# Performance work log

Measured on AMD Instinct MI355X. Metric: run time of the kernel, lower is better.

Reference implementation:

```python
import jax, jax.numpy as jnp
import numpy as np

BN_EPS = 1e-5
NUM_HEADS = 4

def conv1x1_bn_silu(x, w, gamma, beta, mean, var):
    # x: (B,C,H,W), w: (Cout,Cin) -- 1x1 conv, no bias; BN in eval mode; SiLU act
    y = jnp.einsum('bchw,oc->bohw', x, w)
    g = (gamma / jnp.sqrt(var + BN_EPS))[:, None, None]
    b = (beta - mean * gamma / jnp.sqrt(var + BN_EPS))[:, None, None]
    y = y * g + b
    return y * jax.nn.sigmoid(y)

def setup_inputs() -> dict:
    key = jax.random.key(0)
    ks = jax.random.split(key, 16)
    B, H, W, C = 4, 64, 64, 256
    N = H * W
    Ckv = C // 4 * 2  # kv conv out channels = 128
    inp = {
        'x': jax.random.normal(ks[0], (B, N, C), jnp.float32),
        'y': jax.random.normal(ks[1], (B, N, C), jnp.float32),
        'H': H,
        'W': W,
        'q_w': jax.random.normal(ks[2], (C, C), jnp.float32) * (1.0 / np.sqrt(C)),
        'q_gamma': jax.random.uniform(ks[3], (C,), jnp.float32) + 0.5,
        'q_beta': jax.random.normal(ks[4], (C,), jnp.float32) * 0.1,
        'q_mean': jax.random.normal(ks[5], (C,), jnp.float32) * 0.1,
        'q_var': jax.random.uniform(ks[6], (C,), jnp.float32) + 0.5,
        'kv_w': jax.random.normal(ks[7], (Ckv, C), jnp.float32) * (1.0 / np.sqrt(C)),
        'kv_gamma': jax.random.uniform(ks[8], (Ckv,), jnp.float32) + 0.5,
        'kv_beta': jax.random.normal(ks[9], (Ckv,), jnp.float32) * 0.1,
        'kv_mean': jax.random.normal(ks[10], (Ckv,), jnp.float32) * 0.1,
        'kv_var': jax.random.uniform(ks[11], (Ckv,), jnp.float32) + 0.5,
        'proj_w': jax.random.normal(ks[12], (C, C), jnp.float32) * (1.0 / np.sqrt(C)),
        'proj_b': jax.random.normal(ks[13], (C,), jnp.float32) * 0.1,
    }
    return inp

def reference(x, y, H, W, q_w, q_gamma, q_beta, q_mean, q_var,
              kv_w, kv_gamma, kv_beta, kv_mean, kv_var, proj_w, proj_b):
    B, N, C = x.shape
    nh = NUM_HEADS
    hd = C // nh
    scale = hd ** -0.5
    x4 = x.reshape(B, C, H, W)
    y4 = y.reshape(B, C, H, W)
    # q: (B,C,H,W) -> raw reshape (B,N,nh,hd) -> (B,nh,N,hd)  (faithful to torch code)
    q = conv1x1_bn_silu(x4, q_w, q_gamma, q_beta, q_mean, q_var)
    q = q.reshape(B, N, nh, hd).transpose(0, 2, 1, 3)
    # kv: (B,C/2,H,W) -> raw reshape (B,M,2,nh,hd), M = N//4
    kv = conv1x1_bn_silu(y4, kv_w, kv_gamma, kv_beta, kv_mean, kv_var)
    kv = kv.reshape(B, -1, 2, nh, hd).transpose(2, 0, 3, 1, 4)
    k, v = kv[0], kv[1]  # (B,nh,M,hd)
    attn = jnp.einsum('bhnd,bhmd->bhnm', q * scale, k)  # (B,nh,N,M)
    att_map = jax.nn.softmax(attn, axis=-1)
    out = jnp.einsum('bhnm,bhmd->bhnd', att_map, v)  # (B,nh,N,hd)
    out = out.reshape(B, N, C)  # raw reshape, faithful to original
    out = out @ proj_w.T + proj_b
    return out
```

## Files before the change

kernel.cpp:

```cpp
#include <hip/hip_runtime.h>
#include <hip/hip_bf16.h>
#include <math.h>

#define BB 4
#define NTOK 4096
#define CC 256
#define NH 4
#define HD 64
#define CKV 128

typedef _Float16 half8 __attribute__((ext_vector_type(8)));
typedef _Float16 half4 __attribute__((ext_vector_type(4)));
typedef _Float16 half2v __attribute__((ext_vector_type(2)));
typedef float    f32x4 __attribute__((ext_vector_type(4)));
typedef unsigned int uint2v __attribute__((ext_vector_type(2)));

__device__ __forceinline__ half2v pkrtz(float a, float b) {
  return __builtin_bit_cast(half2v, __builtin_amdgcn_cvt_pkrtz(a, b));
}
__device__ __forceinline__ float exp2_fast(float x) {
  float r;
  asm("v_exp_f32 %0, %1" : "=v"(r) : "v"(x));
  return r;
}
__device__ __forceinline__ int swzi(int row, int d) {
  return row * 64 + (d ^ ((row & 7) << 3));
}
__device__ __forceinline__ int swzv(int row, int d) {
  return row * 64 + (d ^ (((row >> 1) & 7) << 3));
}
__device__ __forceinline__ f32x4 mfma16(half8 a, half8 b, f32x4 c) {
  return __builtin_amdgcn_mfma_f32_16x16x32_f16(a, b, c, 0, 0, 0);
}

__global__ __launch_bounds__(256) void pre_all(
    const float* __restrict__ x, const float* __restrict__ y,
    const float* __restrict__ qw, const float* __restrict__ qg_, const float* __restrict__ qb,
    const float* __restrict__ qm, const float* __restrict__ qv,
    const float* __restrict__ kw, const float* __restrict__ kg_, const float* __restrict__ kb,
    const float* __restrict__ km, const float* __restrict__ kvv,
    const float* __restrict__ pw,
    _Float16* __restrict__ Xt, _Float16* __restrict__ Yt,
    _Float16* __restrict__ qWh, float* __restrict__ qB2,
    _Float16* __restrict__ kWh, float* __restrict__ kB2,
    _Float16* __restrict__ pWh)
{
  const int id = blockIdx.x;
  __shared__ float T[64][65];
  const int t = threadIdx.x;
  if (id < 2048) {
    const float* X   = (id < 1024) ? x  : y;
    _Float16*   XT   = (id < 1024) ? Xt : Yt;
    const int i = id & 1023;
    const int pt = i & 63, ct = (i >> 6) & 3, b = i >> 8;
    const float* Xb = X + (size_t)b * CC * NTOK + (size_t)ct * 64 * NTOK + pt * 64;
    const int cr = t >> 4, pc = (t & 15) * 4;
    #pragma unroll
    for (int k = 0; k < 4; ++k) {
      float4 v = *(const float4*)&Xb[(size_t)(cr + k * 16) * NTOK + pc];
      T[cr + k * 16][pc]     = v.x;  T[cr + k * 16][pc + 1] = v.y;
      T[cr + k * 16][pc + 2] = v.z;  T[cr + k * 16][pc + 3] = v.w;
    }
    __syncthreads();
    _Float16* Ot = XT + (size_t)b * NTOK * CC + (size_t)(pt * 64) * CC + ct * 64;
    #pragma unroll
    for (int k = 0; k < 2; ++k) {
      int u = t + k * 256;
      int p = u >> 3, ch = u & 7;
      half8 h;
      #pragma unroll
      for (int j = 0; j < 8; ++j) h[j] = (_Float16)T[ch * 8 + j][p];
      *(half8*)&Ot[(size_t)p * CC + ch * 8] = h;
    }
  } else {
    const int r = id - 2048;
    const int c = t;
    if (r < 256) {
      float g = qg_[r] * rsqrtf(qv[r] + 1e-5f);
      qWh[r * 256 + c] = (_Float16)(qw[r * 256 + c] * g);
      if (c == 0) qB2[r] = qb[r] - qm[r] * g;
    } else if (r < 384) {
      int o = r - 256;
      float g = kg_[o] * rsqrtf(kvv[o] + 1e-5f);
      kWh[o * 256 + c] = (_Float16)(kw[o * 256 + c] * g);
      if (c == 0) kB2[o] = kb[o] - km[o] * g;
    } else if (r < 640) {
      int o = r - 384;
      pWh[o * 256 + c] = (_Float16)pw[o * 256 + c];
    }
  }
}

__global__ __launch_bounds__(256) void conv_mfma_all(
    const _Float16* __restrict__ Xt, const _Float16* __restrict__ Yt,
    const _Float16* __restrict__ qWh, const float* __restrict__ qB2,
    const _Float16* __restrict__ kWh, const float* __restrict__ kB2,
    _Float16* __restrict__ qout, _Float16* __restrict__ kvout)
{
  const int ptile = blockIdx.x, oy = blockIdx.y, b = blockIdx.z;
  const bool isq = oy < 4;
  const _Float16* A  = isq ? Xt : Yt;
  const _Float16* W  = isq ? qWh : kWh;
  const float*    B2 = isq ? qB2 : kB2;
  _Float16*       Y  = isq ? qout : kvout;
  const int otile = isq ? oy : oy - 4;
  const int COUT  = isq ? 256 : 128;

  __shared__ _Float16 Xs[128 * 64];
  __shared__ _Float16 Ws[64 * 64];
  const int t = threadIdx.x, wave = t >> 6, lane = t & 63;
  const int lm = lane & 15, lg = lane >> 4;
  const _Float16* Xb = A + (size_t)b * NTOK * CC + (size_t)ptile * 128 * CC;
  const _Float16* Wb = W + otile * 64 * 256;
  f32x4 acc[2][4];
  #pragma unroll
  for (int m = 0; m < 2; ++m)
    #pragma unroll
    for (int n = 0; n < 4; ++n) acc[m][n] = (f32x4){0.f, 0.f, 0.f, 0.f};

  for (int c0 = 0; c0 < 256; c0 += 64) {
    __syncthreads();
    #pragma unroll
    for (int i = 0; i < 4; ++i) {
      int u = t + i * 256; int p = u >> 3, ch = u & 7;
      *(half8*)&Xs[swzi(p, ch * 8)] = *(const half8*)&Xb[(size_t)p * 256 + c0 + ch * 8];
    }
    #pragma unroll
    for (int i = 0; i < 2; ++i) {
      int u = t + i * 256; int o = u >> 3, ch = u & 7;
      *(half8*)&Ws[swzi(o, ch * 8)] = *(const half8*)&Wb[o * 256 + c0 + ch * 8];
    }
    __syncthreads();
    #pragma unroll
    for (int kh = 0; kh < 2; ++kh) {
      half8 af[2], bf[4];
      #pragma unroll
      for (int m = 0; m < 2; ++m) af[m] = *(half8*)&Xs[swzi(wave * 32 + m * 16 + lm, kh * 32 + lg * 8)];
      #pragma unroll
      for (int n = 0; n < 4; ++n) bf[n] = *(half8*)&Ws[swzi(n * 16 + lm, kh * 32 + lg * 8)];
      #pragma unroll
      for (int m = 0; m < 2; ++m)
        #pragma unroll
        for (int n = 0; n < 4; ++n)
          acc[m][n] = mfma16(af[m], bf[n], acc[m][n]);
    }
  }
  _Float16* Yb = Y + (size_t)b * COUT * NTOK;
  #pragma unroll
  for (int m = 0; m < 2; ++m)
    #pragma unroll
    for (int n = 0; n < 4; ++n) {
      int o = otile * 64 + n * 16 + lm;
      float b2 = B2[o];
      float r[4];
      #pragma unroll
      for (int rr = 0; rr < 4; ++rr) {
        float v = acc[m][n][rr] + b2;
        r[rr] = v / (1.f + __expf(-v));
      }
      half2v p0 = pkrtz(r[0], r[1]);
      half2v p1 = pkrtz(r[2], r[3]);
      half4 h; h[0]=p0[0]; h[1]=p0[1]; h[2]=p1[0]; h[3]=p1[1];
      int p = ptile * 128 + wave * 32 + m * 16 + lg * 4;
      *(half4*)&Yb[(size_t)o * NTOK + p] = h;
    }
}

__global__ __launch_bounds__(512) void attn_mfma5(
    const _Float16* __restrict__ Q,
    const _Float16* __restrict__ KV,
    _Float16* __restrict__ O)
{
  const int nt = blockIdx.x, hh = blockIdx.y, b = blockIdx.z;
  const int n0 = nt * 128;
  const int t = threadIdx.x, wave = t >> 6, lane = t & 63;
  const int lm = lane & 15, lg = lane >> 4;
  const int wq = wave * 16;
  const float SCL = 0.125f * 1.44269504f;

  __shared__ _Float16 Kl[2][64 * 64];
  __shared__ _Float16 Vt[2][64 * 64];
  __shared__ _Float16 Pl[128 * 64];

  const _Float16* Qb  = Q  + (size_t)b * (CC * NTOK)  + hh * 64;
  const _Float16* KVb = KV + (size_t)b * (CKV * NTOK) + hh * 64;

  half8 qf[2];
  {
    int n = n0 + wq + lm;
    const _Float16* src = Qb + (n >> 4) * 4096 + (n & 15) * 256;
    qf[0] = *(const half8*)(src + lg * 8);
    qf[1] = *(const half8*)(src + 32 + lg * 8);
  }

  half8 ones;
  #pragma unroll
  for (int j = 0; j < 8; ++j) ones[j] = (_Float16)1.f;

  f32x4 acc[4], accl;
  float m_run = -1e30f;
  #pragma unroll
  for (int dg = 0; dg < 4; ++dg) acc[dg] = (f32x4){0.f, 0.f, 0.f, 0.f};
  accl = (f32x4){0.f, 0.f, 0.f, 0.f};

  const int kkey = t >> 3, kch = t & 7;
  const int dvp = (t & 31) * 2, kgv = t >> 5;
  const _Float16* kp = KVb + (size_t)(kkey >> 3) * 4096 + (kkey & 7) * 512 + kch * 8;
  const _Float16* vp = KVb + (size_t)(kgv >> 1) * 4096 + (kgv & 1) * 4 * 512 + 256 + dvp;

  half8 kreg;
  unsigned int vreg[4];

  auto PREFETCH = [&]() {
    kreg = *(const half8*)kp;
    #pragma unroll
    for (int j = 0; j < 4; ++j)
      vreg[j] = *(const unsigned int*)(vp + j * 512);
    kp += 8 * 4096;
    vp += 8 * 4096;
  };
  auto STORE_LDS = [&](int buf) {
    *(half8*)&Kl[buf][swzi(kkey, kch * 8)] = kreg;
    unsigned int lo0 = (vreg[0] & 0xffffu) | (vreg[1] << 16);
    unsigned int lo1 = (vreg[2] & 0xffffu) | (vreg[3] << 16);
    unsigned int hi0 = (vreg[0] >> 16) | (vreg[1] & 0xffff0000u);
    unsigned int hi1 = (vreg[2] >> 16) | (vreg[3] & 0xffff0000u);
    *(uint2v*)&Vt[buf][swzv(dvp,     kgv * 4)] = (uint2v){lo0, lo1};
    *(uint2v*)&Vt[buf][swzv(dvp + 1, kgv * 4)] = (uint2v){hi0, hi1};
  };

  PREFETCH();
  STORE_LDS(0);
  __syncthreads();

  int cur = 0;
  for (int mt = 0; mt < 16; ++mt) {
    if (mt < 15) PREFETCH();

    f32x4 sc[4];
    #pragma unroll
    for (int kt = 0; kt < 4; ++kt) {
      half8 kf0 = *(half8*)&Kl[cur][swzi(kt * 16 + lm, lg * 8)];
      half8 kf1 = *(half8*)&Kl[cur][swzi(kt * 16 + lm, 32 + lg * 8)];
      f32x4 z = (f32x4){0.f, 0.f, 0.f, 0.f};
      z = mfma16(kf0, qf[0], z);
      z = mfma16(kf1, qf[1], z);
      sc[kt] = z;
    }

    float t0 = fmaxf(fmaxf(sc[0][0], sc[0][1]), sc[0][2]);
    float t1 = fmaxf(fmaxf(sc[0][3], sc[1][0]), sc[1][1]);
    float t2 = fmaxf(fmaxf(sc[1][2], sc[1][3]), sc[2][0]);
    float t3 = fmaxf(fmaxf(sc[2][1], sc[2][2]), sc[2][3]);
    float t4 = fmaxf(fmaxf(sc[3][0], sc[3][1]), sc[3][2]);
    float tm = fmaxf(fmaxf(fmaxf(t0, t1), t2), fmaxf(fmaxf(t3, t4), sc[3][3]));
    tm *= SCL;
    tm = fmaxf(tm, __shfl_xor(tm, 16, 64));
    tm = fmaxf(tm, __shfl_xor(tm, 32, 64));
    if (__any(tm > m_run + 8.0f)) {
      float mnew = fmaxf(m_run, tm);
      float corr = exp2_fast(m_run - mnew);
      #pragma unroll
      for (int dg = 0; dg < 4; ++dg) acc[dg] *= corr;
      accl *= corr;
      m_run = mnew;
    }
    int qrow = wq + lm;
    #pragma unroll
    for (int kt = 0; kt < 4; ++kt) {
      float p0 = exp2_fast(fmaf(sc[kt][0], SCL, -m_run));
      float p1 = exp2_fast(fmaf(sc[kt][1], SCL, -m_run));
      float p2 = exp2_fast(fmaf(sc[kt][2], SCL, -m_run));
      float p3 = exp2_fast(fmaf(sc[kt][3], SCL, -m_run));
      half2v a = pkrtz(p0, p1), c = pkrtz(p2, p3);
      half4 h; h[0]=a[0]; h[1]=a[1]; h[2]=c[0]; h[3]=c[1];
      *(half4*)&Pl[swzi(qrow, kt * 16 + lg * 4)] = h;
    }

    #pragma unroll
    for (int ka = 0; ka < 2; ++ka) {
      half8 pf = *(half8*)&Pl[swzi(wq + lm, ka * 32 + lg * 8)];
      accl = mfma16(ones, pf, accl);
      #pragma unroll
      for (int dg = 0; dg < 4; ++dg) {
        half8 vf = *(half8*)&Vt[cur][swzv(dg * 16 + lm, ka * 32 + lg * 8)];
        acc[dg] = mfma16(vf, pf, acc[dg]);
      }
    }

    if (mt < 15) STORE_LDS(cur ^ 1);
    __syncthreads();
    cur ^= 1;
  }

  float inv = 1.f / accl[0];
  int n = n0 + wq + lm;
  _Float16* dst = O + ((size_t)(b * NH + hh) * NTOK + n) * 64;
  #pragma unroll
  for (int dg = 0; dg < 4; ++dg) {
    half2v p0 = pkrtz(acc[dg][0] * inv, acc[dg][1] * inv);
    half2v p1 = pkrtz(acc[dg][2] * inv, acc[dg][3] * inv);
    half4 h; h[0]=p0[0]; h[1]=p0[1]; h[2]=p1[0]; h[3]=p1[1];
    *(half4*)(dst + dg * 16 + lg * 4) = h;
  }
}

__global__ __launch_bounds__(256) void proj_mfma(
    const _Float16* __restrict__ A, const _Float16* __restrict__ Wp,
    const float* __restrict__ bias, float* __restrict__ Out)
{
  const int rtile = blockIdx.x, ctile = blockIdx.y;
  __shared__ _Float16 As[128 * 64];
  __shared__ _Float16 Ws[64 * 64];
  const int t = threadIdx.x, wave = t >> 6, lane = t & 63;
  const int lm = lane & 15, lg = lane >> 4;
  const _Float16* Ab = A + (size_t)rtile * 128 * 256;
  const _Float16* Wb = Wp + ctile * 64 * 256;
  f32x4 acc[2][4];
  #pragma unroll
  for (int m = 0; m < 2; ++m)
    #pragma unroll
    for (int n = 0; n < 4; ++n) acc[m][n] = (f32x4){0.f, 0.f, 0.f, 0.f};

  for (int c0 = 0; c0 < 256; c0 += 64) {
    __syncthreads();
    #pragma unroll
    for (int i = 0; i < 4; ++i) {
      int u = t + i * 256; int r = u >> 3, ch = u & 7;
      *(half8*)&As[swzi(r, ch * 8)] = *(const half8*)&Ab[(size_t)r * 256 + c0 + ch * 8];
    }
    #pragma unroll
    for (int i = 0; i < 2; ++i) {
      int u = t + i * 256; int o = u >> 3, ch = u & 7;
      *(half8*)&Ws[swzi(o, ch * 8)] = *(const half8*)&Wb[o * 256 + c0 + ch * 8];
    }
    __syncthreads();
    #pragma unroll
    for (int kh = 0; kh < 2; ++kh) {
      half8 af[2], bf[4];
      #pragma unroll
      for (int m = 0; m < 2; ++m) af[m] = *(half8*)&As[swzi(wave * 32 + m * 16 + lm, kh * 32 + lg * 8)];
      #pragma unroll
      for (int n = 0; n < 4; ++n) bf[n] = *(half8*)&Ws[swzi(n * 16 + lm, kh * 32 + lg * 8)];
      #pragma unroll
      for (int m = 0; m < 2; ++m)
        #pragma unroll
        for (int n = 0; n < 4; ++n)
          acc[m][n] = mfma16(af[m], bf[n], acc[m][n]);
    }
  }
  float* Ob = Out + (size_t)rtile * 128 * 256 + ctile * 64;
  #pragma unroll
  for (int n = 0; n < 4; ++n) {
    float bia = bias[ctile * 64 + n * 16 + lm];
    #pragma unroll
    for (int m = 0; m < 2; ++m)
      #pragma unroll
      for (int rr = 0; rr < 4; ++rr)
        Ob[(size_t)(wave * 32 + m * 16 + lg * 4 + rr) * 256 + n * 16 + lm] =
            acc[m][n][rr] + bia;
  }
}

extern "C" void kernel_launch(void* const* d_in, const int* in_sizes, int n_in,
                              void* d_out, int out_size, void* d_ws, size_t ws_size,
                              hipStream_t stream) {
  const float* x        = (const float*)d_in[0];
  const float* y        = (const float*)d_in[1];
  const float* q_w      = (const float*)d_in[4];
  const float* q_gamma  = (const float*)d_in[5];
  const float* q_beta   = (const float*)d_in[6];
  const float* q_mean   = (const float*)d_in[7];
  const float* q_var    = (const float*)d_in[8];
  const float* kv_w     = (const float*)d_in[9];
  const float* kv_gamma = (const float*)d_in[10];
  const float* kv_beta  = (const float*)d_in[11];
  const float* kv_mean  = (const float*)d_in[12];
  const float* kv_var   = (const float*)d_in[13];
  const float* proj_w   = (const float*)d_in[14];
  const float* proj_b   = (const float*)d_in[15];
  float* out = (float*)d_out;

  _Float16* Xt   = (_Float16*)d_ws;
  _Float16* Yt   = Xt   + (size_t)BB * NTOK * CC;
  _Float16* qbn  = Yt   + (size_t)BB * NTOK * CC;
  _Float16* kvbn = qbn  + (size_t)BB * CC * NTOK;
  _Float16* aout = kvbn + (size_t)BB * CKV * NTOK;
  _Float16* qWh  = aout + (size_t)BB * NH * NTOK * HD;
  _Float16* kWh  = qWh + 256 * 256;
  _Float16* pWh  = kWh + 128 * 256;
  float* qB2 = (float*)(pWh + 256 * 256);
  float* kB2 = qB2 + 256;

  pre_all<<<2688, 256, 0, stream>>>(
      x, y, q_w, q_gamma, q_beta, q_mean, q_var,
      kv_w, kv_gamma, kv_beta, kv_mean, kv_var, proj_w,
      Xt, Yt, qWh, qB2, kWh, kB2, pWh);
  conv_mfma_all<<<dim3(32, 6, BB), 256, 0, stream>>>(
      Xt, Yt, qWh, qB2, kWh, kB2, qbn, kvbn);
  attn_mfma5<<<dim3(32, NH, BB), 512, 0, stream>>>(qbn, kvbn, aout);
  proj_mfma<<<dim3(128, 4), 256, 0, stream>>>(aout, pWh, proj_b, out);
}
```

Before: 66.01 us.

## Process two query tiles per wave in attention to reuse K/V fragments

Each wave now handles 32 query rows instead of 16, so the attention block drops from 512 to 256 threads while keeping 128 queries per block. Each K and V fragment read from LDS now feeds two MFMAs, halving LDS reads per unit of compute, and each thread loads twice as much K/V per prefetch. s_setprio hints are also placed around the MFMA sections. The cost is higher register pressure and fewer waves to hide latency.

```diff
diff --git a/kernel.cpp b/kernel.cpp
--- a/kernel.cpp
+++ b/kernel.cpp
@@ -166,7 +166,7 @@
     }
 }
 
-__global__ __launch_bounds__(512) void attn_mfma5(
+__global__ __launch_bounds__(256) void attn_mfma6(
     const _Float16* __restrict__ Q,
     const _Float16* __restrict__ KV,
     _Float16* __restrict__ O)
@@ -175,7 +175,7 @@
   const int n0 = nt * 128;
   const int t = threadIdx.x, wave = t >> 6, lane = t & 63;
   const int lm = lane & 15, lg = lane >> 4;
-  const int wq = wave * 16;
+  const int wq = wave * 32;
   const float SCL = 0.125f * 1.44269504f;
 
   __shared__ _Float16 Kl[2][64 * 64];
@@ -185,48 +185,57 @@
   const _Float16* Qb  = Q  + (size_t)b * (CC * NTOK)  + hh * 64;
   const _Float16* KVb = KV + (size_t)b * (CKV * NTOK) + hh * 64;
 
-  half8 qf[2];
-  {
-    int n = n0 + wq + lm;
+  half8 qf[2][2];
+  #pragma unroll
+  for (int qg = 0; qg < 2; ++qg) {
+    int n = n0 + wq + qg * 16 + lm;
     const _Float16* src = Qb + (n >> 4) * 4096 + (n & 15) * 256;
-    qf[0] = *(const half8*)(src + lg * 8);
-    qf[1] = *(const half8*)(src + 32 + lg * 8);
+    qf[qg][0] = *(const half8*)(src + lg * 8);
+    qf[qg][1] = *(const half8*)(src + 32 + lg * 8);
   }
 
   half8 ones;
   #pragma unroll
   for (int j = 0; j < 8; ++j) ones[j] = (_Float16)1.f;
 
-  f32x4 acc[4], accl;
-  float m_run = -1e30f;
-  #pragma unroll
-  for (int dg = 0; dg < 4; ++dg) acc[dg] = (f32x4){0.f, 0.f, 0.f, 0.f};
-  accl = (f32x4){0.f, 0.f, 0.f, 0.f};
-
-  const int kkey = t >> 3, kch = t & 7;
+  f32x4 acc[2][4], accl[2];
+  float m_run[2];
+  #pragma unroll
+  for (int qg = 0; qg < 2; ++qg) {
+    m_run[qg] = -1e30f;
+    accl[qg] = (f32x4){0.f, 0.f, 0.f, 0.f};
+    #pragma unroll
+    for (int dg = 0; dg < 4; ++dg) acc[qg][dg] = (f32x4){0.f, 0.f, 0.f, 0.f};
+  }
+
+  const int kkey = t >> 2, kch = (t & 3) * 2;
   const int dvp = (t & 31) * 2, kgv = t >> 5;
   const _Float16* kp = KVb + (size_t)(kkey >> 3) * 4096 + (kkey & 7) * 512 + kch * 8;
-  const _Float16* vp = KVb + (size_t)(kgv >> 1) * 4096 + (kgv & 1) * 4 * 512 + 256 + dvp;
-
-  half8 kreg;
-  unsigned int vreg[4];
+  const _Float16* vp = KVb + (size_t)kgv * 4096 + 256 + dvp;
+
+  half8 kreg[2];
+  unsigned int vreg[8];
 
   auto PREFETCH = [&]() {
-    kreg = *(const half8*)kp;
-    #pragma unroll
-    for (int j = 0; j < 4; ++j)
+    kreg[0] = *(const half8*)kp;
+    kreg[1] = *(const half8*)(kp + 8);
+    #pragma unroll
+    for (int j = 0; j < 8; ++j)
       vreg[j] = *(const unsigned int*)(vp + j * 512);
     kp += 8 * 4096;
     vp += 8 * 4096;
   };
   auto STORE_LDS = [&](int buf) {
-    *(half8*)&Kl[buf][swzi(kkey, kch * 8)] = kreg;
-    unsigned int lo0 = (vreg[0] & 0xffffu) | (vreg[1] << 16);
-    unsigned int lo1 = (vreg[2] & 0xffffu) | (vreg[3] << 16);
-    unsigned int hi0 = (vreg[0] >> 16) | (vreg[1] & 0xffff0000u);
-    unsigned int hi1 = (vreg[2] >> 16) | (vreg[3] & 0xffff0000u);
-    *(uint2v*)&Vt[buf][swzv(dvp,     kgv * 4)] = (uint2v){lo0, lo1};
-    *(uint2v*)&Vt[buf][swzv(dvp + 1, kgv * 4)] = (uint2v){hi0, hi1};
+    *(half8*)&Kl[buf][swzi(kkey, kch * 8)]       = kreg[0];
+    *(half8*)&Kl[buf][swzi(kkey, kch * 8 + 8)]   = kreg[1];
+    half8 lo, hi;
+    #pragma unroll
+    for (int j = 0; j < 8; ++j) {
+      half2v hv = __builtin_bit_cast(half2v, vreg[j]);
+      lo[j] = hv[0]; hi[j] = hv[1];
+    }
+    *(half8*)&Vt[buf][swzv(dvp,     kgv * 8)] = lo;
+    *(half8*)&Vt[buf][swzv(dvp + 1, kgv * 8)] = hi;
   };
 
   PREFETCH();
@@ -237,71 +246,90 @@
   for (int mt = 0; mt < 16; ++mt) {
     if (mt < 15) PREFETCH();
 
-    f32x4 sc[4];
+    f32x4 sc[2][4];
+    __builtin_amdgcn_s_setprio(1);
     #pragma unroll
     for (int kt = 0; kt < 4; ++kt) {
       half8 kf0 = *(half8*)&Kl[cur][swzi(kt * 16 + lm, lg * 8)];
       half8 kf1 = *(half8*)&Kl[cur][swzi(kt * 16 + lm, 32 + lg * 8)];
-      f32x4 z = (f32x4){0.f, 0.f, 0.f, 0.f};
-      z = mfma16(kf0, qf[0], z);
-      z = mfma16(kf1, qf[1], z);
-      sc[kt] = z;
-    }
-
-    float t0 = fmaxf(fmaxf(sc[0][0], sc[0][1]), sc[0][2]);
-    float t1 = fmaxf(fmaxf(sc[0][3], sc[1][0]), sc[1][1]);
-    float t2 = fmaxf(fmaxf(sc[1][2], sc[1][3]), sc[2][0]);
-    float t3 = fmaxf(fmaxf(sc[2][1], sc[2][2]), sc[2][3]);
-    float t4 = fmaxf(fmaxf(sc[3][0], sc[3][1]), sc[3][2]);
-    float tm = fmaxf(fmaxf(fmaxf(t0, t1), t2), fmaxf(fmaxf(t3, t4), sc[3][3]));
-    tm *= SCL;
-    tm = fmaxf(tm, __shfl_xor(tm, 16, 64));
-    tm = fmaxf(tm, __shfl_xor(tm, 32, 64));
-    if (__any(tm > m_run + 8.0f)) {
-      float mnew = fmaxf(m_run, tm);
-      float corr = exp2_fast(m_run - mnew);
-      #pragma unroll
-      for (int dg = 0; dg < 4; ++dg) acc[dg] *= corr;
-      accl *= corr;
-      m_run = mnew;
-    }
-    int qrow = wq + lm;
-    #pragma unroll
-    for (int kt = 0; kt < 4; ++kt) {
-      float p0 = exp2_fast(fmaf(sc[kt][0], SCL, -m_run));
-      float p1 = exp2_fast(fmaf(sc[kt][1], SCL, -m_run));
-      float p2 = exp2_fast(fmaf(sc[kt][2], SCL, -m_run));
-      float p3 = exp2_fast(fmaf(sc[kt][3], SCL, -m_run));
-      half2v a = pkrtz(p0, p1), c = pkrtz(p2, p3);
-      half4 h; h[0]=a[0]; h[1]=a[1]; h[2]=c[0]; h[3]=c[1];
-      *(half4*)&Pl[swzi(qrow, kt * 16 + lg * 4)] = h;
-    }
-
+      #pragma unroll
+      for (int qg = 0; qg < 2; ++qg) {
+        f32x4 z = (f32x4){0.f, 0.f, 0.f, 0.f};
+        z = mfma16(kf0, qf[qg][0], z);
+        z = mfma16(kf1, qf[qg][1], z);
+        sc[qg][kt] = z;
+      }
+    }
+    __builtin_amdgcn_s_setprio(0);
+
+    #pragma unroll
+    for (int qg = 0; qg < 2; ++qg) {
+      float t0 = fmaxf(fmaxf(sc[qg][0][0], sc[qg][0][1]), sc[qg][0][2]);
+      float t1 = fmaxf(fmaxf(sc[qg][0][3], sc[qg][1][0]), sc[qg][1][1]);
+      float t2 = fmaxf(fmaxf(sc[qg][1][2], sc[qg][1][3]), sc[qg][2][0]);
+      float t3 = fmaxf(fmaxf(sc[qg][2][1], sc[qg][2][2]), sc[qg][2][3]);
+      float t4 = fmaxf(fmaxf(sc[qg][3][0], sc[qg][3][1]), sc[qg][3][2]);
+      float tm = fmaxf(fmaxf(fmaxf(t0, t1), t2), fmaxf(fmaxf(t3, t4), sc[qg][3][3]));
+      tm *= SCL;
+      tm = fmaxf(tm, __shfl_xor(tm, 16, 64));
+      tm = fmaxf(tm, __shfl_xor(tm, 32, 64));
+      if (__any(tm > m_run[qg] + 8.0f)) {
+        float mnew = fmaxf(m_run[qg], tm);
+        float corr = exp2_fast(m_run[qg] - mnew);
+        #pragma unroll
+        for (int dg = 0; dg < 4; ++dg) acc[qg][dg] *= corr;
+        accl[qg] *= corr;
+        m_run[qg] = mnew;
+      }
+      int qrow = wq + qg * 16 + lm;
+      #pragma unroll
+      for (int kt = 0; kt < 4; ++kt) {
+        float p0 = exp2_fast(fmaf(sc[qg][kt][0], SCL, -m_run[qg]));
+        float p1 = exp2_fast(fmaf(sc[qg][kt][1], SCL, -m_run[qg]));
+        float p2 = exp2_fast(fmaf(sc[qg][kt][2], SCL, -m_run[qg]));
+        float p3 = exp2_fast(fmaf(sc[qg][kt][3], SCL, -m_run[qg]));
+        half2v a = pkrtz(p0, p1), c = pkrtz(p2, p3);
+        half4 h; h[0]=a[0]; h[1]=a[1]; h[2]=c[0]; h[3]=c[1];
+        *(half4*)&Pl[swzi(qrow, kt * 16 + lg * 4)] = h;
+      }
+    }
+
+    __builtin_amdgcn_s_setprio(1);
     #pragma unroll
     for (int ka = 0; ka < 2; ++ka) {
-      half8 pf = *(half8*)&Pl[swzi(wq + lm, ka * 32 + lg * 8)];
-      accl = mfma16(ones, pf, accl);
+      half8 pf[2];
+      #pragma unroll
+      for (int qg = 0; qg < 2; ++qg) {
+        pf[qg] = *(half8*)&Pl[swzi(wq + qg * 16 + lm, ka * 32 + lg * 8)];
+        accl[qg] = mfma16(ones, pf[qg], accl[qg]);
+      }
       #pragma unroll
       for (int dg = 0; dg < 4; ++dg) {
         half8 vf = *(half8*)&Vt[cur][swzv(dg * 16 + lm, ka * 32 + lg * 8)];
-        acc[dg] = mfma16(vf, pf, acc[dg]);
-      }
-    }
+        #pragma unroll
+        for (int qg = 0; qg < 2; ++qg)
+          acc[qg][dg] = mfma16(vf, pf[qg], acc[qg][dg]);
+      }
+    }
+    __builtin_amdgcn_s_setprio(0);
 
     if (mt < 15) STORE_LDS(cur ^ 1);
     __syncthreads();
     cur ^= 1;
   }
 
-  float inv = 1.f / accl[0];
-  int n = n0 + wq + lm;
-  _Float16* dst = O + ((size_t)(b * NH + hh) * NTOK + n) * 64;
-  #pragma unroll
-  for (int dg = 0; dg < 4; ++dg) {
-    half2v p0 = pkrtz(acc[dg][0] * inv, acc[dg][1] * inv);
-    half2v p1 = pkrtz(acc[dg][2] * inv, acc[dg][3] * inv);
-    half4 h; h[0]=p0[0]; h[1]=p0[1]; h[2]=p1[0]; h[3]=p1[1];
-    *(half4*)(dst + dg * 16 + lg * 4) = h;
+  #pragma unroll
+  for (int qg = 0; qg < 2; ++qg) {
+    float inv = 1.f / accl[qg][0];
+    int n = n0 + wq + qg * 16 + lm;
+    _Float16* dst = O + ((size_t)(b * NH + hh) * NTOK + n) * 64;
+    #pragma unroll
+    for (int dg = 0; dg < 4; ++dg) {
+      half2v p0 = pkrtz(acc[qg][dg][0] * inv, acc[qg][dg][1] * inv);
+      half2v p1 = pkrtz(acc[qg][dg][2] * inv, acc[qg][dg][3] * inv);
+      half4 h; h[0]=p0[0]; h[1]=p0[1]; h[2]=p1[0]; h[3]=p1[1];
+      *(half4*)(dst + dg * 16 + lg * 4) = h;
+    }
   }
 }
 
@@ -398,6 +426,6 @@
       Xt, Yt, qWh, qB2, kWh, kB2, pWh);
   conv_mfma_all<<<dim3(32, 6, BB), 256, 0, stream>>>(
       Xt, Yt, qWh, qB2, kWh, kB2, qbn, kvbn);
-  attn_mfma5<<<dim3(32, NH, BB), 512, 0, stream>>>(qbn, kvbn, aout);
+  attn_mfma6<<<dim3(32, NH, BB), 256, 0, stream>>>(qbn, kvbn, aout);
   proj_mfma<<<dim3(128, 4), 256, 0, stream>>>(aout, pWh, proj_b, out);
 }
```

After: 67.07 us. About the same (+1.6%).
